# Kernel optimization log

Measured on AMD Instinct MI355X. Metric: run time of the kernel, lower is better.

## Reference

```python
import jax, jax.numpy as jnp
import numpy as np

B, T, I, H, C = 8192, 28, 28, 128, 10


def setup_inputs() -> dict:
    key = jax.random.key(0)
    ks = jax.random.split(key, 7)
    s_ih = 1.0 / np.sqrt(H)
    return {
        "x": jax.random.normal(ks[0], (B, T, I), dtype=jnp.float32),
        "W_ih": jax.random.normal(ks[1], (4 * H, I), dtype=jnp.float32) * s_ih,
        "W_hh": jax.random.normal(ks[2], (4 * H, H), dtype=jnp.float32) * s_ih,
        "b_ih": jax.random.normal(ks[3], (4 * H,), dtype=jnp.float32) * s_ih,
        "b_hh": jax.random.normal(ks[4], (4 * H,), dtype=jnp.float32) * s_ih,
        "W_fc": jax.random.normal(ks[5], (C, H), dtype=jnp.float32) * s_ih,
        "b_fc": jnp.zeros((C,), dtype=jnp.float32),
    }


def reference(x, W_ih, W_hh, b_ih, b_hh, W_fc, b_fc):
    # x: [B, T, I]. PyTorch LSTM gate order: i, f, g, o.
    b = b_ih + b_hh  # [4H]
    # Precompute input projections for all timesteps: [T, B, 4H]
    x_proj = jnp.einsum("bti,gi->tbg", x, W_ih) + b
    h0 = jnp.zeros((x.shape[0], H), dtype=x.dtype)
    c0 = jnp.zeros_like(h0)

    def step(carry, xp_t):
        h, c = carry
        gates = xp_t + h @ W_hh.T  # [B, 4H]
        i_g, f_g, g_g, o_g = jnp.split(gates, 4, axis=-1)
        i_g = jax.nn.sigmoid(i_g)
        f_g = jax.nn.sigmoid(f_g)
        g_g = jnp.tanh(g_g)
        o_g = jax.nn.sigmoid(o_g)
        c = f_g * c + i_g * g_g
        h = o_g * jnp.tanh(c)
        return (h, c), None

    (h_last, _), _ = jax.lax.scan(step, (h0, c0), x_proj)
    # outputs[:, -1, :] == final hidden state; fc + relu
    return jax.nn.relu(h_last @ W_fc.T + b_fc)
```

## Files before the change

kernel.cpp:

```cpp
#include <hip/hip_runtime.h>
#include <math.h>

typedef __attribute__((ext_vector_type(8))) _Float16 half8;
typedef __attribute__((ext_vector_type(4))) _Float16 half4;
typedef __attribute__((ext_vector_type(4))) float    f32x4;

#define TSTEPS 28
#define IDIM   28
#define HDIM   128
#define NKC    5
#define TILE_B 16
#define CDIM   10

#if __has_builtin(__builtin_amdgcn_exp2f)
#define EXP2F(x) __builtin_amdgcn_exp2f(x)
#else
#define EXP2F(x) exp2f(x)
#endif
#if __has_builtin(__builtin_amdgcn_rcpf)
#define RCPF(x) __builtin_amdgcn_rcpf(x)
#else
#define RCPF(x) (1.0f / (x))
#endif

#define NLOG2E (-1.44269504f)
#define P2LOG2E (2.88539008f)

__global__ __launch_bounds__(256) void pack_w(const float* __restrict__ Wih,
                                              const float* __restrict__ Whh,
                                              _Float16* __restrict__ P) {
    int e = blockIdx.x * 256 + threadIdx.x;
    if (e >= NKC * 4 * 8 * 64 * 8) return;
    int j  = e & 7;
    int ln = (e >> 3) & 63;
    int w  = (e >> 9) & 7;
    int t  = (e >> 12) & 3;
    int kc = e >> 14;
    int k  = kc * 32 + ((ln >> 4) << 3) + j;
    int u  = w * 16 + (ln & 15);
    int g  = t * HDIM + u;
    float v = 0.f;
    if (k < HDIM)              v = Whh[g * HDIM + k];
    else if (k < HDIM + IDIM)  v = Wih[g * IDIM + (k - HDIM)];
    float sc = (t == 2) ? P2LOG2E : NLOG2E;
    P[e] = (_Float16)(v * sc);
}

__global__ __launch_bounds__(512, 4) void lstm_kernel(
    const float* __restrict__ x,
    const _Float16* __restrict__ P,
    const float* __restrict__ b_ih, const float* __restrict__ b_hh,
    const float* __restrict__ Wfc,
    const float* __restrict__ b_fc,
    float* __restrict__ out)
{
    __shared__ __align__(16) _Float16 frag[2][NKC][64][8];
    __shared__ __align__(16) _Float16 Plds[4][8][64][8];
    __shared__ __align__(16) float hplain[TILE_B][HDIM + 4];

    const int tid = threadIdx.x;
    const int l   = tid & 63;
    const int w   = tid >> 6;
    const int b0  = blockIdx.x * TILE_B;
    const int u   = w * 16 + (l & 15);

    {
        const float4* P4 = (const float4*)P;
        float4* dst = (float4*)Plds;
        #pragma unroll
        for (int q = 0; q < 4; ++q)
            dst[tid + q * 512] = P4[8192 + tid + q * 512];
    }
    half8 breg[4][4];
    {
        const half8* Pp = (const half8*)P;
        #pragma unroll
        for (int kc = 0; kc < 4; ++kc)
            #pragma unroll
            for (int t4 = 0; t4 < 4; ++t4)
                breg[t4][kc] = Pp[((kc * 4 + t4) * 8 + w) * 64 + l];
    }
    float biasv[4];
    #pragma unroll
    for (int t4 = 0; t4 < 4; ++t4) {
        float sc = (t4 == 2) ? P2LOG2E : NLOG2E;
        biasv[t4] = (b_ih[t4 * HDIM + u] + b_hh[t4 * HDIM + u]) * sc;
    }

    {
        float4 z = {0.f, 0.f, 0.f, 0.f};
        if (tid < 256) ((float4*)&frag[0][0][0][0])[tid] = z;
        if (tid < 32) {
            int b = tid >> 4, i = tid & 15;
            half4 zh = {(_Float16)0.f, (_Float16)0.f, (_Float16)0.f, (_Float16)0.f};
            *(half4*)&frag[b][4][48 + i][4] = zh;
        }
    }
    const int xrow = tid / 7, xg = tid % 7;
    if (tid < 112) {
        float4 xv = ((const float4*)(x + ((size_t)(b0 + xrow) * TSTEPS + 0) * IDIM))[xg];
        half4 hv = {(_Float16)xv.x, (_Float16)xv.y, (_Float16)xv.z, (_Float16)xv.w};
        *(half4*)&frag[0][4][xrow + 16 * (xg >> 1)][(xg & 1) * 4] = hv;
    }

    float cst[4] = {0.f, 0.f, 0.f, 0.f};
    const int kc_h = w >> 1;
    const int quad = (2 * w + ((l >> 3) & 1)) & 3;
    const int jh   = l & 7;

    __syncthreads();

    auto step = [&](int t, _Float16 (*cur)[64][8], _Float16 (*nxt)[64][8]) {
        float4 xv;
        const bool doload = (t + 1 < TSTEPS) && (tid < 112);
        if (doload)
            xv = ((const float4*)(x + ((size_t)(b0 + xrow) * TSTEPS + (t + 1)) * IDIM))[xg];

        f32x4 acc[4];
        #pragma unroll
        for (int t4 = 0; t4 < 4; ++t4) {
            f32x4 a4 = {biasv[t4], biasv[t4], biasv[t4], biasv[t4]};
            acc[t4] = a4;
        }

        #pragma unroll
        for (int kc = 0; kc < NKC; ++kc) {
            half8 a = *(const half8*)&cur[kc][l][0];
            if (kc < 4) {
                acc[0] = __builtin_amdgcn_mfma_f32_16x16x32_f16(a, breg[0][kc], acc[0], 0, 0, 0);
                acc[1] = __builtin_amdgcn_mfma_f32_16x16x32_f16(a, breg[1][kc], acc[1], 0, 0, 0);
                acc[2] = __builtin_amdgcn_mfma_f32_16x16x32_f16(a, breg[2][kc], acc[2], 0, 0, 0);
                acc[3] = __builtin_amdgcn_mfma_f32_16x16x32_f16(a, breg[3][kc], acc[3], 0, 0, 0);
            } else {
                #pragma unroll
                for (int t4 = 0; t4 < 4; ++t4) {
                    half8 b = *(const half8*)&Plds[t4][w][l][0];
                    acc[t4] = __builtin_amdgcn_mfma_f32_16x16x32_f16(a, b, acc[t4], 0, 0, 0);
                }
            }
        }

        #pragma unroll
        for (int r = 0; r < 4; ++r) {
            int m = ((l >> 4) << 2) + r;
            float is = RCPF(1.f + EXP2F(acc[0][r]));
            float fs = RCPF(1.f + EXP2F(acc[1][r]));
            float os = RCPF(1.f + EXP2F(acc[3][r]));
            float gt = 1.f - 2.f * RCPF(1.f + EXP2F(acc[2][r]));
            float c  = fs * cst[r] + is * gt;
            cst[r] = c;
            float tc = 1.f - 2.f * RCPF(1.f + EXP2F(c * P2LOG2E));
            float h  = os * tc;
            nxt[kc_h][m + 16 * quad][jh] = (_Float16)h;
            if (t == TSTEPS - 1) hplain[m][u] = h;
        }
        if (doload) {
            half4 hv = {(_Float16)xv.x, (_Float16)xv.y, (_Float16)xv.z, (_Float16)xv.w};
            *(half4*)&nxt[4][xrow + 16 * (xg >> 1)][(xg & 1) * 4] = hv;
        }
        __syncthreads();
    };

    for (int tt = 0; tt < TSTEPS; tt += 2) {
        step(tt,     frag[0], frag[1]);
        step(tt + 1, frag[1], frag[0]);
    }

    if (tid < TILE_B * CDIM) {
        int row = tid / CDIM, c = tid % CDIM;
        const float4* hv = (const float4*)&hplain[row][0];
        const float4* wf = (const float4*)(Wfc + c * HDIM);
        float s = b_fc[c];
        #pragma unroll
        for (int q = 0; q < 32; ++q) {
            float4 a = hv[q], b = wf[q];
            s += a.x * b.x + a.y * b.y + a.z * b.z + a.w * b.w;
        }
        out[(size_t)(b0 + row) * CDIM + c] = fmaxf(s, 0.f);
    }
}

extern "C" void kernel_launch(void* const* d_in, const int* in_sizes, int n_in,
                              void* d_out, int out_size, void* d_ws, size_t ws_size,
                              hipStream_t stream) {
    const float* x   = (const float*)d_in[0];
    const float* Wih = (const float*)d_in[1];
    const float* Whh = (const float*)d_in[2];
    const float* bih = (const float*)d_in[3];
    const float* bhh = (const float*)d_in[4];
    const float* Wfc = (const float*)d_in[5];
    const float* bfc = (const float*)d_in[6];
    float* out = (float*)d_out;
    _Float16* P = (_Float16*)d_ws;

    hipLaunchKernelGGL(pack_w, dim3(320), dim3(256), 0, stream, Wih, Whh, P);
    hipLaunchKernelGGL(lstm_kernel, dim3(8192 / TILE_B), dim3(512), 0, stream,
                       x, P, bih, bhh, Wfc, bfc, out);
}
```

Measured before the change: 127.5 us.

## Fold bias into MFMA, share reciprocals in gates, stagger block start

The combined bias, scaled in fp16, is packed into the spare K column of the input chunk, and a constant 1 is placed in the x fragment so the MFMA adds it. This removes the per-thread bias registers and the accumulator initialisation. Gate activations pair sigmoids so that two reciprocals serve four gates, and all A fragments are loaded before the MFMA chain, which is now reordered per gate. Launch bounds drop from 4 to 2 waves per SIMD to allow more registers, and blocks with bit 256 set sleep briefly at start to stagger their phases. Storing the bias in fp16 loses some precision, and multiplying two denominators risks overflow when the exponentials are large.

```diff
diff --git a/kernel.cpp b/kernel.cpp
--- a/kernel.cpp
+++ b/kernel.cpp
@@ -28,6 +28,8 @@
 
 __global__ __launch_bounds__(256) void pack_w(const float* __restrict__ Wih,
                                               const float* __restrict__ Whh,
+                                              const float* __restrict__ bih,
+                                              const float* __restrict__ bhh,
                                               _Float16* __restrict__ P) {
     int e = blockIdx.x * 256 + threadIdx.x;
     if (e >= NKC * 4 * 8 * 64 * 8) return;
@@ -40,16 +42,16 @@
     int u  = w * 16 + (ln & 15);
     int g  = t * HDIM + u;
     float v = 0.f;
-    if (k < HDIM)              v = Whh[g * HDIM + k];
-    else if (k < HDIM + IDIM)  v = Wih[g * IDIM + (k - HDIM)];
+    if (k < HDIM)                   v = Whh[g * HDIM + k];
+    else if (k < HDIM + IDIM)       v = Wih[g * IDIM + (k - HDIM)];
+    else if (k == HDIM + IDIM)      v = bih[g] + bhh[g];
     float sc = (t == 2) ? P2LOG2E : NLOG2E;
     P[e] = (_Float16)(v * sc);
 }
 
-__global__ __launch_bounds__(512, 4) void lstm_kernel(
+__global__ __launch_bounds__(512, 2) void lstm_kernel(
     const float* __restrict__ x,
     const _Float16* __restrict__ P,
-    const float* __restrict__ b_ih, const float* __restrict__ b_hh,
     const float* __restrict__ Wfc,
     const float* __restrict__ b_fc,
     float* __restrict__ out)
@@ -62,7 +64,6 @@
     const int l   = tid & 63;
     const int w   = tid >> 6;
     const int b0  = blockIdx.x * TILE_B;
-    const int u   = w * 16 + (l & 15);
 
     {
         const float4* P4 = (const float4*)P;
@@ -80,21 +81,15 @@
             for (int t4 = 0; t4 < 4; ++t4)
                 breg[t4][kc] = Pp[((kc * 4 + t4) * 8 + w) * 64 + l];
     }
-    float biasv[4];
-    #pragma unroll
-    for (int t4 = 0; t4 < 4; ++t4) {
-        float sc = (t4 == 2) ? P2LOG2E : NLOG2E;
-        biasv[t4] = (b_ih[t4 * HDIM + u] + b_hh[t4 * HDIM + u]) * sc;
+
+    if (tid < 256) {
+        float4 z = {0.f, 0.f, 0.f, 0.f};
+        ((float4*)&frag[0][0][0][0])[tid] = z;
     }
-
-    {
-        float4 z = {0.f, 0.f, 0.f, 0.f};
-        if (tid < 256) ((float4*)&frag[0][0][0][0])[tid] = z;
-        if (tid < 32) {
-            int b = tid >> 4, i = tid & 15;
-            half4 zh = {(_Float16)0.f, (_Float16)0.f, (_Float16)0.f, (_Float16)0.f};
-            *(half4*)&frag[b][4][48 + i][4] = zh;
-        }
+    if (tid < 32) {
+        int b = tid >> 4, i = tid & 15;
+        half4 onev = {(_Float16)1.f, (_Float16)0.f, (_Float16)0.f, (_Float16)0.f};
+        *(half4*)&frag[b][4][48 + i][4] = onev;
     }
     const int xrow = tid / 7, xg = tid % 7;
     if (tid < 112) {
@@ -104,55 +99,60 @@
     }
 
     float cst[4] = {0.f, 0.f, 0.f, 0.f};
+    const int u    = w * 16 + (l & 15);
     const int kc_h = w >> 1;
     const int quad = (2 * w + ((l >> 3) & 1)) & 3;
     const int jh   = l & 7;
 
     __syncthreads();
 
-    auto step = [&](int t, _Float16 (*cur)[64][8], _Float16 (*nxt)[64][8]) {
+#if __has_builtin(__builtin_amdgcn_s_sleep)
+    if (blockIdx.x & 256) __builtin_amdgcn_s_sleep(25);
+#endif
+
+    auto step = [&](int t, const _Float16 (*cur)[64][8], _Float16 (*nxt)[64][8]) {
+        const bool last = (t == TSTEPS - 1);
         float4 xv;
         const bool doload = (t + 1 < TSTEPS) && (tid < 112);
         if (doload)
             xv = ((const float4*)(x + ((size_t)(b0 + xrow) * TSTEPS + (t + 1)) * IDIM))[xg];
 
+        half8 a[NKC];
+        #pragma unroll
+        for (int kc = 0; kc < NKC; ++kc)
+            a[kc] = *(const half8*)&cur[kc][l][0];
+
         f32x4 acc[4];
         #pragma unroll
         for (int t4 = 0; t4 < 4; ++t4) {
-            f32x4 a4 = {biasv[t4], biasv[t4], biasv[t4], biasv[t4]};
-            acc[t4] = a4;
-        }
-
-        #pragma unroll
-        for (int kc = 0; kc < NKC; ++kc) {
-            half8 a = *(const half8*)&cur[kc][l][0];
-            if (kc < 4) {
-                acc[0] = __builtin_amdgcn_mfma_f32_16x16x32_f16(a, breg[0][kc], acc[0], 0, 0, 0);
-                acc[1] = __builtin_amdgcn_mfma_f32_16x16x32_f16(a, breg[1][kc], acc[1], 0, 0, 0);
-                acc[2] = __builtin_amdgcn_mfma_f32_16x16x32_f16(a, breg[2][kc], acc[2], 0, 0, 0);
-                acc[3] = __builtin_amdgcn_mfma_f32_16x16x32_f16(a, breg[3][kc], acc[3], 0, 0, 0);
-            } else {
-                #pragma unroll
-                for (int t4 = 0; t4 < 4; ++t4) {
-                    half8 b = *(const half8*)&Plds[t4][w][l][0];
-                    acc[t4] = __builtin_amdgcn_mfma_f32_16x16x32_f16(a, b, acc[t4], 0, 0, 0);
-                }
-            }
+            f32x4 z = {0.f, 0.f, 0.f, 0.f};
+            acc[t4] = z;
+            #pragma unroll
+            for (int kc = 0; kc < 4; ++kc)
+                acc[t4] = __builtin_amdgcn_mfma_f32_16x16x32_f16(a[kc], breg[t4][kc], acc[t4], 0, 0, 0);
+            half8 b = *(const half8*)&Plds[t4][w][l][0];
+            acc[t4] = __builtin_amdgcn_mfma_f32_16x16x32_f16(a[4], b, acc[t4], 0, 0, 0);
         }
 
         #pragma unroll
         for (int r = 0; r < 4; ++r) {
-            int m = ((l >> 4) << 2) + r;
-            float is = RCPF(1.f + EXP2F(acc[0][r]));
-            float fs = RCPF(1.f + EXP2F(acc[1][r]));
-            float os = RCPF(1.f + EXP2F(acc[3][r]));
-            float gt = 1.f - 2.f * RCPF(1.f + EXP2F(acc[2][r]));
+            float Ei = EXP2F(acc[0][r]);
+            float Ef = EXP2F(acc[1][r]);
+            float Eg = EXP2F(acc[2][r]);
+            float Eo = EXP2F(acc[3][r]);
+            float Di = 1.f + Ei, Df = 1.f + Ef, Dg = 1.f + Eg, Do = 1.f + Eo;
+            float Rif = RCPF(Di * Df);
+            float Rgo = RCPF(Dg * Do);
+            float is = Rif * Df, fs = Rif * Di;
+            float gt = 1.f - 2.f * (Rgo * Do);
+            float os = Rgo * Dg;
             float c  = fs * cst[r] + is * gt;
             cst[r] = c;
             float tc = 1.f - 2.f * RCPF(1.f + EXP2F(c * P2LOG2E));
             float h  = os * tc;
+            int m = ((l >> 4) << 2) + r;
             nxt[kc_h][m + 16 * quad][jh] = (_Float16)h;
-            if (t == TSTEPS - 1) hplain[m][u] = h;
+            if (last) hplain[m][u] = h;
         }
         if (doload) {
             half4 hv = {(_Float16)xv.x, (_Float16)xv.y, (_Float16)xv.z, (_Float16)xv.w};
@@ -173,8 +173,8 @@
         float s = b_fc[c];
         #pragma unroll
         for (int q = 0; q < 32; ++q) {
-            float4 a = hv[q], b = wf[q];
-            s += a.x * b.x + a.y * b.y + a.z * b.z + a.w * b.w;
+            float4 a4 = hv[q], b4 = wf[q];
+            s += a4.x * b4.x + a4.y * b4.y + a4.z * b4.z + a4.w * b4.w;
         }
         out[(size_t)(b0 + row) * CDIM + c] = fmaxf(s, 0.f);
     }
@@ -193,7 +193,7 @@
     float* out = (float*)d_out;
     _Float16* P = (_Float16*)d_ws;
 
-    hipLaunchKernelGGL(pack_w, dim3(320), dim3(256), 0, stream, Wih, Whh, P);
+    hipLaunchKernelGGL(pack_w, dim3(320), dim3(256), 0, stream, Wih, Whh, bih, bhh, P);
     hipLaunchKernelGGL(lstm_kernel, dim3(8192 / TILE_B), dim3(512), 0, stream,
-                       x, P, bih, bhh, Wfc, bfc, out);
+                       x, P, Wfc, bfc, out);
 }
```

Result: no change. 125.7 us (-1.4%).
